# Kernel tuning notes

Measured on AMD Instinct MI355X. Metric: run time of the kernel, lower is better.

Reference implementation:

```python
import jax, jax.numpy as jnp
import numpy as np

B, C, N, K, CO = 16, 256, 16384, 64, 512
EPS_NORM = 1e-12
BN_EPS = 1e-5


def _l2norm(v, axis):
    n = jnp.sqrt(jnp.sum(v * v, axis=axis, keepdims=True))
    return v / jnp.maximum(n, EPS_NORM)


def setup_inputs() -> dict:
    key = jax.random.key(0)
    ks = jax.random.split(key, 8)
    x = jax.random.normal(ks[0], (B, C, N), dtype=jnp.float32)
    # NetVLAD assignment conv: Conv1d(C, K, k=1) -> weight (K, C), bias (K)
    assign_w = jax.random.normal(ks[1], (K, C), dtype=jnp.float32) / np.sqrt(C)
    assign_b = jax.random.normal(ks[2], (K,), dtype=jnp.float32) / np.sqrt(C)
    centroids = jax.random.uniform(ks[3], (K, C), dtype=jnp.float32)
    # reduct_feat Conv1d(K*C, CO, k=1): weight (CO, K*C), bias (CO)
    red_w = jax.random.normal(ks[4], (CO, K * C), dtype=jnp.float32) * np.sqrt(2.0 / (K * C))
    red_b = jnp.zeros((CO,), dtype=jnp.float32)
    bn_w = jnp.ones((CO,), dtype=jnp.float32)
    bn_b = jnp.zeros((CO,), dtype=jnp.float32)
    return {"x": x, "assign_w": assign_w, "assign_b": assign_b,
            "centroids": centroids, "red_w": red_w, "red_b": red_b,
            "bn_w": bn_w, "bn_b": bn_b}


def reference(x, assign_w, assign_b, centroids, red_w, red_b, bn_w, bn_b):
    # --- NetVLAD ---
    xn = _l2norm(x, axis=1)                                   # (B,C,N) L2 over channel
    logits = jnp.einsum('kc,bcn->bkn', assign_w, xn) + assign_b[None, :, None]
    a = jax.nn.softmax(logits, axis=1)                        # (B,K,N) soft assignment
    # residual aggregation reformulated: sum_n a*(x - c) = (a @ x^T) - sum_n(a) * c
    agg = jnp.einsum('bkn,bcn->bkc', a, xn)                   # (B,K,C)
    a_sum = jnp.sum(a, axis=2)                                # (B,K)
    vlad = agg - a_sum[:, :, None] * centroids[None, :, :]    # (B,K,C)
    vlad = _l2norm(vlad, axis=2)                              # intra-norm over C
    vlad = vlad.reshape(B, K * C)
    vlad = _l2norm(vlad, axis=1)                              # global L2
    # --- reduct_feat: 1x1 conv on length-1 sequence ---
    y = vlad @ red_w.T + red_b                                # (B,CO)
    # BatchNorm1d, training mode: stats over batch (L=1), biased variance
    mean = jnp.mean(y, axis=0)
    var = jnp.mean((y - mean) ** 2, axis=0)
    y = bn_w * (y - mean) / jnp.sqrt(var + BN_EPS) + bn_b
    y = jax.nn.relu(y)
    return y[:, :, None]                                      # (B,CO,1)
```

## Files before the change

### kernel.cpp

```cpp
#include <hip/hip_runtime.h>
#include <math.h>

#define B_   16
#define C_   256
#define N_   16384
#define K_   64
#define CO_  512

typedef __attribute__((ext_vector_type(8))) short short8;
typedef __attribute__((ext_vector_type(4))) float floatx4;

__device__ inline unsigned short f2bf(float f) {
    unsigned int u = __float_as_uint(f);
    u = (u + 0x7FFFu + ((u >> 16) & 1u)) >> 16;
    return (unsigned short)u;
}
__device__ inline float bf2f(unsigned short h) {
    return __uint_as_float(((unsigned int)h) << 16);
}

__global__ __launch_bounds__(512, 4) void k1_assign_agg(
    const float* __restrict__ x, const float* __restrict__ aw,
    const float* __restrict__ ab, float* __restrict__ agg,
    float* __restrict__ asum)
{
    __shared__ __align__(16) unsigned char smem[81152];
    unsigned short* x_cn  = (unsigned short*)smem;
    unsigned short* x_nc  = (unsigned short*)(smem + 36864);
    unsigned short* a_ld  = (unsigned short*)(smem + 70656);
    unsigned short* colsq = (unsigned short*)(smem + 79872);
    float* rnorm = (float*)(smem + 79872);
    float* part  = (float*)(smem + 79872 + 256);
    float* red   = part;

    const int t    = threadIdx.x;
    const int lane = t & 63;
    const int wav  = t >> 6;
    const int b    = blockIdx.x >> 5;
    const int tile = blockIdx.x & 31;
    const float* xb = x + (size_t)b * ((size_t)C_ * N_) + tile * 512;

    const int j16 = lane & 15;
    const int g4  = lane >> 4;
    const int mw  = wav & 3;
    const int jw  = wav >> 2;

    short8 wf[8];
    {
        const float* wrow = aw + (mw * 16 + j16) * 256 + g4 * 8;
        #pragma unroll
        for (int ki = 0; ki < 8; ++ki) {
            const float* p = wrow + ki * 32;
            short8 f;
            #pragma unroll
            for (int i = 0; i < 8; ++i) f[i] = (short)f2bf(p[i]);
            wf[ki] = f;
        }
    }
    const float4 abf = *(const float4*)(ab + mw * 16 + g4 * 4);

    floatx4 acc[4][2];
    #pragma unroll
    for (int m = 0; m < 4; ++m)
        #pragma unroll
        for (int c2 = 0; c2 < 2; ++c2)
            acc[m][c2] = (floatx4){0.f, 0.f, 0.f, 0.f};
    float asr[4] = {0.f, 0.f, 0.f, 0.f};

    const int nL = t & 63;
    const int cg = t >> 6;

    for (int chunk = 0; chunk < 8; ++chunk) {
        const int n0 = chunk * 64;
        __syncthreads();
        {
            const float* src = xb + n0 + nL;
            unsigned int* nc_row = (unsigned int*)(x_nc + nL * 264);
            float sq = 0.f;
            #pragma unroll
            for (int i = 0; i < 16; ++i) {
                int c0 = cg * 32 + 2 * i;
                float f0 = src[(size_t)c0 * N_];
                float f1 = src[(size_t)(c0 + 1) * N_];
                sq += f0 * f0 + f1 * f1;
                unsigned int h0 = f2bf(f0), h1 = f2bf(f1);
                x_cn[c0 * 72 + nL]       = (unsigned short)h0;
                x_cn[(c0 + 1) * 72 + nL] = (unsigned short)h1;
                nc_row[cg * 16 + i] = h0 | (h1 << 16);
            }
            colsq[nL * 8 + cg] = f2bf(sq);
        }
        __syncthreads();
        if (t < 64) {
            short8 cs = *(const short8*)(colsq + t * 8);
            float s = 0.f;
            #pragma unroll
            for (int i = 0; i < 8; ++i) s += bf2f((unsigned short)cs[i]);
            rnorm[t] = 1.0f / fmaxf(sqrtf(s), 1e-12f);
        }
        __syncthreads();
        floatx4 ct0 = {0.f, 0.f, 0.f, 0.f}, ct1 = {0.f, 0.f, 0.f, 0.f};
        {
            const unsigned short* r0 = x_nc + (jw * 32 + j16) * 264 + g4 * 8;
            const unsigned short* r1 = r0 + 16 * 264;
            #pragma unroll
            for (int ki = 0; ki < 8; ++ki) {
                short8 b0 = *(const short8*)(r0 + ki * 32);
                short8 b1 = *(const short8*)(r1 + ki * 32);
                ct0 = __builtin_amdgcn_mfma_f32_16x16x32_bf16(wf[ki], b0, ct0, 0, 0, 0);
                ct1 = __builtin_amdgcn_mfma_f32_16x16x32_bf16(wf[ki], b1, ct1, 0, 0, 0);
            }
        }
        const float rn0 = rnorm[jw * 32 + j16];
        const float rn1 = rnorm[jw * 32 + 16 + j16];
        float e0[4], e1[4];
        float p0 = 0.f, p1 = 0.f;
        #pragma unroll
        for (int r = 0; r < 4; ++r) {
            float l0 = ct0[r] * rn0 + ((const float*)&abf)[r];
            float l1 = ct1[r] * rn1 + ((const float*)&abf)[r];
            e0[r] = __expf(l0); e1[r] = __expf(l1);
            p0 += e0[r]; p1 += e1[r];
        }
        p0 += __shfl_xor(p0, 16); p0 += __shfl_xor(p0, 32);
        p1 += __shfl_xor(p1, 16); p1 += __shfl_xor(p1, 32);
        if (lane < 16) {
            part[(jw * 32 + j16) * 4 + mw]      = p0;
            part[(jw * 32 + 16 + j16) * 4 + mw] = p1;
        }
        __syncthreads();
        {
            float4 q0 = *(const float4*)(part + (jw * 32 + j16) * 4);
            float4 q1 = *(const float4*)(part + (jw * 32 + 16 + j16) * 4);
            float i0 = 1.0f / (q0.x + q0.y + q0.z + q0.w);
            float i1 = 1.0f / (q1.x + q1.y + q1.z + q1.w);
            float s0 = rn0 * i0, s1 = rn1 * i1;
            unsigned short* arow = a_ld + (mw * 16 + g4 * 4) * 72;
            #pragma unroll
            for (int r = 0; r < 4; ++r) {
                arow[r * 72 + jw * 32 + j16]      = f2bf(e0[r] * s0);
                arow[r * 72 + jw * 32 + 16 + j16] = f2bf(e1[r] * s1);
                asr[r] += e0[r] * i0 + e1[r] * i1;
            }
        }
        __syncthreads();
        {
            const int cb = wav * 32;
            #pragma unroll
            for (int ki = 0; ki < 2; ++ki) {
                const int nn = ki * 32 + g4 * 8;
                short8 af[4];
                #pragma unroll
                for (int m = 0; m < 4; ++m)
                    af[m] = *(const short8*)(a_ld + (m * 16 + j16) * 72 + nn);
                #pragma unroll
                for (int c2 = 0; c2 < 2; ++c2) {
                    short8 bfv = *(const short8*)(x_cn + (cb + c2 * 16 + j16) * 72 + nn);
                    #pragma unroll
                    for (int m = 0; m < 4; ++m)
                        acc[m][c2] = __builtin_amdgcn_mfma_f32_16x16x32_bf16(af[m], bfv, acc[m][c2], 0, 0, 0);
                }
            }
        }
    }

    __syncthreads();
    #pragma unroll
    for (int r = 0; r < 4; ++r) {
        asr[r] += __shfl_xor(asr[r], 1);
        asr[r] += __shfl_xor(asr[r], 2);
        asr[r] += __shfl_xor(asr[r], 4);
        asr[r] += __shfl_xor(asr[r], 8);
    }
    if (j16 == 0) {
        #pragma unroll
        for (int r = 0; r < 4; ++r) red[wav * 16 + g4 * 4 + r] = asr[r];
    }
    __syncthreads();
    if (t < 64) {
        float s = red[(t >> 4) * 16 + (t & 15)] + red[((t >> 4) + 4) * 16 + (t & 15)];
        atomicAdd(&asum[b * 64 + t], s);
    }
    #pragma unroll
    for (int m = 0; m < 4; ++m)
        #pragma unroll
        for (int c2 = 0; c2 < 2; ++c2)
            #pragma unroll
            for (int r = 0; r < 4; ++r) {
                int k = m * 16 + g4 * 4 + r;
                int c = wav * 32 + c2 * 16 + j16;
                atomicAdd(&agg[((size_t)(b * 64 + k)) * 256 + c], acc[m][c2][r]);
            }
}

__global__ void k2a_vlad_norm(const float* __restrict__ agg,
                              const float* __restrict__ asum,
                              const float* __restrict__ cent,
                              float* __restrict__ vn,
                              float* __restrict__ gsq)
{
    const int b = blockIdx.x >> 6;
    const int k = blockIdx.x & 63;
    const int lane = threadIdx.x;
    const float as = asum[b * 64 + k];
    float v[4];
    float sq = 0.f;
    #pragma unroll
    for (int i = 0; i < 4; ++i) {
        int c = lane + 64 * i;
        v[i] = agg[((size_t)(b * 64 + k)) * 256 + c] - as * cent[k * 256 + c];
        sq += v[i] * v[i];
    }
    #pragma unroll
    for (int off = 32; off >= 1; off >>= 1) sq += __shfl_xor(sq, off);
    float scale = 1.0f / fmaxf(sqrtf(sq), 1e-12f);
    #pragma unroll
    for (int i = 0; i < 4; ++i) {
        int c = lane + 64 * i;
        vn[(size_t)b * 16384 + k * 256 + c] = v[i] * scale;
    }
    if (lane == 0) atomicAdd(&gsq[b], sq * scale * scale);
}

__global__ __launch_bounds__(256) void k2b_gemm(
    const float* __restrict__ vn, const float* __restrict__ gsq,
    const float* __restrict__ rw, const float* __restrict__ rb,
    float* __restrict__ y)
{
    __shared__ float pr[4][2][16];
    const int t = threadIdx.x;
    const int co0 = blockIdx.x * 2;
    const float4* rw4 = (const float4*)rw;
    const float4* vn4 = (const float4*)vn;
    float a0[16], a1[16];
    #pragma unroll
    for (int bb = 0; bb < 16; ++bb) { a0[bb] = 0.f; a1[bb] = 0.f; }
    for (int it = 0; it < 16; ++it) {
        int idx = it * 256 + t;
        float4 wa = rw4[(size_t)co0 * 4096 + idx];
        float4 wb = rw4[(size_t)(co0 + 1) * 4096 + idx];
        #pragma unroll
        for (int bb = 0; bb < 16; ++bb) {
            float4 v = vn4[(size_t)bb * 4096 + idx];
            a0[bb] += wa.x * v.x + wa.y * v.y + wa.z * v.z + wa.w * v.w;
            a1[bb] += wb.x * v.x + wb.y * v.y + wb.z * v.z + wb.w * v.w;
        }
    }
    #pragma unroll
    for (int off = 32; off >= 1; off >>= 1)
        #pragma unroll
        for (int bb = 0; bb < 16; ++bb) {
            a0[bb] += __shfl_xor(a0[bb], off);
            a1[bb] += __shfl_xor(a1[bb], off);
        }
    const int wav = t >> 6, lane = t & 63;
    if (lane < 16) { pr[wav][0][lane] = a0[lane]; pr[wav][1][lane] = a1[lane]; }
    __syncthreads();
    if (t < 32) {
        int u = t >> 4, bb = t & 15;
        float s = pr[0][u][bb] + pr[1][u][bb] + pr[2][u][bb] + pr[3][u][bb];
        float g = fmaxf(sqrtf(gsq[bb]), 1e-12f);
        y[bb * 512 + co0 + u] = s / g + rb[co0 + u];
    }
}

__global__ void k2c_bn(const float* __restrict__ y,
                       const float* __restrict__ bnw,
                       const float* __restrict__ bnb,
                       float* __restrict__ out)
{
    const int co = threadIdx.x;
    float vals[16];
    float m = 0.f;
    #pragma unroll
    for (int bb = 0; bb < 16; ++bb) {
        vals[bb] = y[bb * 512 + co];
        m += vals[bb];
    }
    m *= (1.0f / 16.0f);
    float var = 0.f;
    #pragma unroll
    for (int bb = 0; bb < 16; ++bb) {
        float d = vals[bb] - m;
        var += d * d;
    }
    var *= (1.0f / 16.0f);
    float inv = 1.0f / sqrtf(var + 1e-5f);
    float w = bnw[co], bias = bnb[co];
    #pragma unroll
    for (int bb = 0; bb < 16; ++bb) {
        float o = w * (vals[bb] - m) * inv + bias;
        out[bb * 512 + co] = fmaxf(o, 0.f);
    }
}

extern "C" void kernel_launch(void* const* d_in, const int* in_sizes, int n_in,
                              void* d_out, int out_size, void* d_ws, size_t ws_size,
                              hipStream_t stream)
{
    const float* x    = (const float*)d_in[0];
    const float* aw   = (const float*)d_in[1];
    const float* ab   = (const float*)d_in[2];
    const float* cent = (const float*)d_in[3];
    const float* rw   = (const float*)d_in[4];
    const float* rb   = (const float*)d_in[5];
    const float* bnw  = (const float*)d_in[6];
    const float* bnb  = (const float*)d_in[7];
    float* out = (float*)d_out;

    char* ws = (char*)d_ws;
    float* agg  = (float*)(ws);
    float* asum = (float*)(ws + 1048576);
    float* gsq  = (float*)(ws + 1052672);
    float* vn   = (float*)(ws + 1056768);
    float* y    = (float*)(ws + 1056768 + 1048576);

    hipMemsetAsync(ws, 0, 1056768, stream);

    hipLaunchKernelGGL(k1_assign_agg, dim3(512), dim3(512), 0, stream,
                       x, aw, ab, agg, asum);
    hipLaunchKernelGGL(k2a_vlad_norm, dim3(B_ * K_), dim3(64), 0, stream,
                       agg, asum, cent, vn, gsq);
    hipLaunchKernelGGL(k2b_gemm, dim3(256), dim3(256), 0, stream,
                       vn, gsq, rw, rb, y);
    hipLaunchKernelGGL(k2c_bn, dim3(1), dim3(512), 0, stream,
                       y, bnw, bnb, out);
}
```

Baseline: 540.4 us.

## Prefetch x into registers, swizzle LDS layouts, and split-K the reduction GEMM

The assignment/aggregation kernel now loads each chunk of x as float2 vectors into registers one chunk ahead, so global loads overlap the MFMA work. LDS tiles are written with XOR swizzles instead of padding, and column squared norms are kept in fp32. The reduction GEMM gives each output channel two blocks that each cover half of K and combine results with atomics. The global-norm scale and bias are applied later in the BN kernel. This trades more registers, atomics and a larger memset for better overlap and more GEMM parallelism.

```diff
diff --git a/kernel.cpp b/kernel.cpp
--- a/kernel.cpp
+++ b/kernel.cpp
@@ -8,29 +8,27 @@
 #define CO_  512
 
 typedef __attribute__((ext_vector_type(8))) short short8;
+typedef __attribute__((ext_vector_type(4))) short short4v;
 typedef __attribute__((ext_vector_type(4))) float floatx4;
 
-__device__ inline unsigned short f2bf(float f) {
+__device__ inline unsigned int f2bf(float f) {
     unsigned int u = __float_as_uint(f);
-    u = (u + 0x7FFFu + ((u >> 16) & 1u)) >> 16;
-    return (unsigned short)u;
-}
-__device__ inline float bf2f(unsigned short h) {
-    return __uint_as_float(((unsigned int)h) << 16);
-}
+    return (u + 0x7FFFu + ((u >> 16) & 1u)) >> 16;
+}
+
 
 __global__ __launch_bounds__(512, 4) void k1_assign_agg(
     const float* __restrict__ x, const float* __restrict__ aw,
     const float* __restrict__ ab, float* __restrict__ agg,
     float* __restrict__ asum)
 {
-    __shared__ __align__(16) unsigned char smem[81152];
-    unsigned short* x_cn  = (unsigned short*)smem;
-    unsigned short* x_nc  = (unsigned short*)(smem + 36864);
-    unsigned short* a_ld  = (unsigned short*)(smem + 70656);
-    unsigned short* colsq = (unsigned short*)(smem + 79872);
-    float* rnorm = (float*)(smem + 79872);
-    float* part  = (float*)(smem + 79872 + 256);
+    __shared__ __align__(16) unsigned char smem[79872];
+    unsigned short* x_cn = (unsigned short*)smem;
+    unsigned short* x_nc = (unsigned short*)(smem + 32768);
+    unsigned short* a_ld = (unsigned short*)(smem + 66048);
+    float* colsq = (float*)(smem + 74240);
+    float* rnorm = (float*)(smem + 78592);
+    float* part  = (float*)(smem + 78848);
     float* red   = part;
 
     const int t    = threadIdx.x;
@@ -44,16 +42,18 @@
     const int g4  = lane >> 4;
     const int mw  = wav & 3;
     const int jw  = wav >> 2;
+    const int p   = t & 31;
+    const int g   = t >> 5;
 
     short8 wf[8];
     {
         const float* wrow = aw + (mw * 16 + j16) * 256 + g4 * 8;
         #pragma unroll
         for (int ki = 0; ki < 8; ++ki) {
-            const float* p = wrow + ki * 32;
+            const float* q = wrow + ki * 32;
             short8 f;
             #pragma unroll
-            for (int i = 0; i < 8; ++i) f[i] = (short)f2bf(p[i]);
+            for (int i = 0; i < 8; ++i) f[i] = (short)f2bf(q[i]);
             wf[ki] = f;
         }
     }
@@ -67,48 +67,73 @@
             acc[m][c2] = (floatx4){0.f, 0.f, 0.f, 0.f};
     float asr[4] = {0.f, 0.f, 0.f, 0.f};
 
-    const int nL = t & 63;
-    const int cg = t >> 6;
+    float2 v[16];
+    {
+        const float* ps = xb + 2 * p;
+        #pragma unroll
+        for (int i = 0; i < 16; ++i)
+            v[i] = *(const float2*)(ps + (size_t)(g * 16 + i) * N_);
+    }
 
     for (int chunk = 0; chunk < 8; ++chunk) {
-        const int n0 = chunk * 64;
-        __syncthreads();
-        {
-            const float* src = xb + n0 + nL;
-            unsigned int* nc_row = (unsigned int*)(x_nc + nL * 264);
-            float sq = 0.f;
-            #pragma unroll
-            for (int i = 0; i < 16; ++i) {
-                int c0 = cg * 32 + 2 * i;
-                float f0 = src[(size_t)c0 * N_];
-                float f1 = src[(size_t)(c0 + 1) * N_];
-                sq += f0 * f0 + f1 * f1;
-                unsigned int h0 = f2bf(f0), h1 = f2bf(f1);
-                x_cn[c0 * 72 + nL]       = (unsigned short)h0;
-                x_cn[(c0 + 1) * 72 + nL] = (unsigned short)h1;
-                nc_row[cg * 16 + i] = h0 | (h1 << 16);
-            }
-            colsq[nL * 8 + cg] = f2bf(sq);
+        __syncthreads();
+        float sq0 = 0.f, sq1 = 0.f;
+        #pragma unroll
+        for (int half = 0; half < 2; ++half) {
+            unsigned int hL[8], hH[8];
+            #pragma unroll
+            for (int i = 0; i < 8; ++i) {
+                float2 vv = v[half * 8 + i];
+                sq0 += vv.x * vv.x; sq1 += vv.y * vv.y;
+                hL[i] = f2bf(vv.x); hH[i] = f2bf(vv.y);
+                int c = g * 16 + half * 8 + i;
+                ((unsigned int*)x_cn)[c * 32 + (((p >> 1) ^ (c & 14)) << 1) + (p & 1)]
+                    = hL[i] | (hH[i] << 16);
+            }
+            unsigned short* r0 = x_nc + (2 * p) * 260 + g * 16 + half * 8;
+            unsigned short* r1 = r0 + 260;
+            uint2 wl0, wl1, wh0, wh1;
+            wl0.x = hL[0] | (hL[1] << 16); wl0.y = hL[2] | (hL[3] << 16);
+            wl1.x = hL[4] | (hL[5] << 16); wl1.y = hL[6] | (hL[7] << 16);
+            wh0.x = hH[0] | (hH[1] << 16); wh0.y = hH[2] | (hH[3] << 16);
+            wh1.x = hH[4] | (hH[5] << 16); wh1.y = hH[6] | (hH[7] << 16);
+            *(uint2*)(r0 + 0) = wl0; *(uint2*)(r0 + 4) = wl1;
+            *(uint2*)(r1 + 0) = wh0; *(uint2*)(r1 + 4) = wh1;
+        }
+        colsq[(2 * p) * 17 + g]     = sq0;
+        colsq[(2 * p + 1) * 17 + g] = sq1;
+        if (chunk < 7) {
+            const float* ps = xb + (chunk + 1) * 64 + 2 * p;
+            #pragma unroll
+            for (int i = 0; i < 16; ++i)
+                v[i] = *(const float2*)(ps + (size_t)(g * 16 + i) * N_);
         }
         __syncthreads();
         if (t < 64) {
-            short8 cs = *(const short8*)(colsq + t * 8);
             float s = 0.f;
             #pragma unroll
-            for (int i = 0; i < 8; ++i) s += bf2f((unsigned short)cs[i]);
+            for (int q = 0; q < 16; ++q) s += colsq[t * 17 + q];
             rnorm[t] = 1.0f / fmaxf(sqrtf(s), 1e-12f);
         }
         __syncthreads();
         floatx4 ct0 = {0.f, 0.f, 0.f, 0.f}, ct1 = {0.f, 0.f, 0.f, 0.f};
         {
-            const unsigned short* r0 = x_nc + (jw * 32 + j16) * 264 + g4 * 8;
-            const unsigned short* r1 = r0 + 16 * 264;
+            const unsigned short* rA0 = x_nc + (jw * 32 + j16) * 260 + g4 * 8;
+            const unsigned short* rA1 = rA0 + 16 * 260;
             #pragma unroll
             for (int ki = 0; ki < 8; ++ki) {
-                short8 b0 = *(const short8*)(r0 + ki * 32);
-                short8 b1 = *(const short8*)(r1 + ki * 32);
-                ct0 = __builtin_amdgcn_mfma_f32_16x16x32_bf16(wf[ki], b0, ct0, 0, 0, 0);
-                ct1 = __builtin_amdgcn_mfma_f32_16x16x32_bf16(wf[ki], b1, ct1, 0, 0, 0);
+                short4v a0 = *(const short4v*)(rA0 + ki * 32);
+                short4v a1 = *(const short4v*)(rA0 + ki * 32 + 4);
+                short4v b0 = *(const short4v*)(rA1 + ki * 32);
+                short4v b1 = *(const short4v*)(rA1 + ki * 32 + 4);
+                short8 f0, f1;
+                #pragma unroll
+                for (int i = 0; i < 4; ++i) {
+                    f0[i] = a0[i]; f0[i + 4] = a1[i];
+                    f1[i] = b0[i]; f1[i + 4] = b1[i];
+                }
+                ct0 = __builtin_amdgcn_mfma_f32_16x16x32_bf16(wf[ki], f0, ct0, 0, 0, 0);
+                ct1 = __builtin_amdgcn_mfma_f32_16x16x32_bf16(wf[ki], f1, ct1, 0, 0, 0);
             }
         }
         const float rn0 = rnorm[jw * 32 + j16];
@@ -135,11 +160,14 @@
             float i0 = 1.0f / (q0.x + q0.y + q0.z + q0.w);
             float i1 = 1.0f / (q1.x + q1.y + q1.z + q1.w);
             float s0 = rn0 * i0, s1 = rn1 * i1;
-            unsigned short* arow = a_ld + (mw * 16 + g4 * 4) * 72;
+            const int n0c = jw * 32 + j16, n1c = n0c + 16;
             #pragma unroll
             for (int r = 0; r < 4; ++r) {
-                arow[r * 72 + jw * 32 + j16]      = f2bf(e0[r] * s0);
-                arow[r * 72 + jw * 32 + 16 + j16] = f2bf(e1[r] * s1);
+                int k = mw * 16 + g4 * 4 + r;
+                a_ld[k * 64 + ((((n0c) >> 2) ^ (k & 14)) << 2) + (n0c & 3)]
+                    = (unsigned short)f2bf(e0[r] * s0);
+                a_ld[k * 64 + ((((n1c) >> 2) ^ (k & 14)) << 2) + (n1c & 3)]
+                    = (unsigned short)f2bf(e1[r] * s1);
                 asr[r] += e0[r] * i0 + e1[r] * i1;
             }
         }
@@ -148,14 +176,17 @@
             const int cb = wav * 32;
             #pragma unroll
             for (int ki = 0; ki < 2; ++ki) {
-                const int nn = ki * 32 + g4 * 8;
+                const int sub = ki * 8 + g4 * 2;
                 short8 af[4];
                 #pragma unroll
-                for (int m = 0; m < 4; ++m)
-                    af[m] = *(const short8*)(a_ld + (m * 16 + j16) * 72 + nn);
+                for (int m = 0; m < 4; ++m) {
+                    int k = m * 16 + j16;
+                    af[m] = *(const short8*)&a_ld[k * 64 + ((sub ^ (k & 14)) << 2)];
+                }
                 #pragma unroll
                 for (int c2 = 0; c2 < 2; ++c2) {
-                    short8 bfv = *(const short8*)(x_cn + (cb + c2 * 16 + j16) * 72 + nn);
+                    int c = cb + c2 * 16 + j16;
+                    short8 bfv = *(const short8*)&x_cn[c * 64 + ((sub ^ (c & 14)) << 2)];
                     #pragma unroll
                     for (int m = 0; m < 4; ++m)
                         acc[m][c2] = __builtin_amdgcn_mfma_f32_16x16x32_bf16(af[m], bfv, acc[m][c2], 0, 0, 0);
@@ -223,58 +254,54 @@
 }
 
 __global__ __launch_bounds__(256) void k2b_gemm(
-    const float* __restrict__ vn, const float* __restrict__ gsq,
-    const float* __restrict__ rw, const float* __restrict__ rb,
+    const float* __restrict__ vn, const float* __restrict__ rw,
     float* __restrict__ y)
 {
-    __shared__ float pr[4][2][16];
+    __shared__ float pr[4][16];
     const int t = threadIdx.x;
-    const int co0 = blockIdx.x * 2;
-    const float4* rw4 = (const float4*)rw;
-    const float4* vn4 = (const float4*)vn;
-    float a0[16], a1[16];
-    #pragma unroll
-    for (int bb = 0; bb < 16; ++bb) { a0[bb] = 0.f; a1[bb] = 0.f; }
-    for (int it = 0; it < 16; ++it) {
+    const int co   = blockIdx.x >> 1;
+    const int half = blockIdx.x & 1;
+    const float4* rwr = (const float4*)rw + (size_t)co * 4096 + half * 2048;
+    const float4* vnb = (const float4*)vn + half * 2048;
+    float a0[16];
+    #pragma unroll
+    for (int bb = 0; bb < 16; ++bb) a0[bb] = 0.f;
+    for (int it = 0; it < 8; ++it) {
         int idx = it * 256 + t;
-        float4 wa = rw4[(size_t)co0 * 4096 + idx];
-        float4 wb = rw4[(size_t)(co0 + 1) * 4096 + idx];
+        float4 w = rwr[idx];
         #pragma unroll
         for (int bb = 0; bb < 16; ++bb) {
-            float4 v = vn4[(size_t)bb * 4096 + idx];
-            a0[bb] += wa.x * v.x + wa.y * v.y + wa.z * v.z + wa.w * v.w;
-            a1[bb] += wb.x * v.x + wb.y * v.y + wb.z * v.z + wb.w * v.w;
+            float4 vv = vnb[(size_t)bb * 4096 + idx];
+            a0[bb] += w.x * vv.x + w.y * vv.y + w.z * vv.z + w.w * vv.w;
         }
     }
     #pragma unroll
     for (int off = 32; off >= 1; off >>= 1)
         #pragma unroll
-        for (int bb = 0; bb < 16; ++bb) {
+        for (int bb = 0; bb < 16; ++bb)
             a0[bb] += __shfl_xor(a0[bb], off);
-            a1[bb] += __shfl_xor(a1[bb], off);
-        }
     const int wav = t >> 6, lane = t & 63;
-    if (lane < 16) { pr[wav][0][lane] = a0[lane]; pr[wav][1][lane] = a1[lane]; }
+    if (lane < 16) pr[wav][lane] = a0[lane];
     __syncthreads();
-    if (t < 32) {
-        int u = t >> 4, bb = t & 15;
-        float s = pr[0][u][bb] + pr[1][u][bb] + pr[2][u][bb] + pr[3][u][bb];
-        float g = fmaxf(sqrtf(gsq[bb]), 1e-12f);
-        y[bb * 512 + co0 + u] = s / g + rb[co0 + u];
-    }
+    if (t < 16)
+        atomicAdd(&y[t * 512 + co], pr[0][t] + pr[1][t] + pr[2][t] + pr[3][t]);
 }
 
 __global__ void k2c_bn(const float* __restrict__ y,
+                       const float* __restrict__ gsq,
+                       const float* __restrict__ rb,
                        const float* __restrict__ bnw,
                        const float* __restrict__ bnb,
                        float* __restrict__ out)
 {
     const int co = threadIdx.x;
+    const float rbv = rb[co];
     float vals[16];
     float m = 0.f;
     #pragma unroll
     for (int bb = 0; bb < 16; ++bb) {
-        vals[bb] = y[bb * 512 + co];
+        float gv = fmaxf(sqrtf(gsq[bb]), 1e-12f);
+        vals[bb] = y[bb * 512 + co] / gv + rbv;
         m += vals[bb];
     }
     m *= (1.0f / 16.0f);
@@ -310,19 +337,19 @@
 
     char* ws = (char*)d_ws;
     float* agg  = (float*)(ws);
-    float* asum = (float*)(ws + 1048576);
-    float* gsq  = (float*)(ws + 1052672);
-    float* vn   = (float*)(ws + 1056768);
-    float* y    = (float*)(ws + 1056768 + 1048576);
-
-    hipMemsetAsync(ws, 0, 1056768, stream);
+    float* asum = (float*)(ws + 0x100000);
+    float* gsq  = (float*)(ws + 0x101000);
+    float* y    = (float*)(ws + 0x102000);
+    float* vn   = (float*)(ws + 0x110000);
+
+    hipMemsetAsync(ws, 0, 0x10A000, stream);
 
     hipLaunchKernelGGL(k1_assign_agg, dim3(512), dim3(512), 0, stream,
                        x, aw, ab, agg, asum);
     hipLaunchKernelGGL(k2a_vlad_norm, dim3(B_ * K_), dim3(64), 0, stream,
                        agg, asum, cent, vn, gsq);
-    hipLaunchKernelGGL(k2b_gemm, dim3(256), dim3(256), 0, stream,
-                       vn, gsq, rw, rb, y);
+    hipLaunchKernelGGL(k2b_gemm, dim3(CO_ * 2), dim3(256), 0, stream,
+                       vn, rw, y);
     hipLaunchKernelGGL(k2c_bn, dim3(1), dim3(512), 0, stream,
-                       y, bnw, bnb, out);
-}
+                       y, gsq, rb, bnw, bnb, out);
+}
```

Measured after the change: 523.5 us. -3.1%, faster.
